# Kernel optimization log

Hardware: AMD Instinct MI355X
Metric: run time of the kernel (lower is better)

The kernel has to match this reference:

```python
import jax, jax.numpy as jnp
import numpy as np

N = 100000   # nodes
E = 3200000  # edges
G = 512      # graphs in batch
EPS = 1e-5   # batchnorm eps


def _lin(key, fan_in, fan_out):
    return jax.random.normal(key, (fan_in, fan_out), jnp.float32) / np.sqrt(fan_in)


def setup_inputs() -> dict:
    key = jax.random.key(0)
    ks = jax.random.split(key, 12)
    x = jax.random.normal(ks[0], (N, 2), jnp.float32)
    edge_index = jax.random.randint(ks[1], (2, E), 0, N, dtype=jnp.int64)
    batch_index = jnp.sort(jax.random.randint(ks[2], (N,), 0, G, dtype=jnp.int64))
    w = (8, 32, 128)
    return {
        "x": x, "edge_index": edge_index, "batch_index": batch_index,
        "W1": _lin(ks[3], 2, w[0]),   "b1": jnp.zeros((w[0],), jnp.float32),
        "g1": jnp.ones((w[0],), jnp.float32),  "be1": jnp.zeros((w[0],), jnp.float32),
        "W2": _lin(ks[4], w[0], w[1]), "b2": jnp.zeros((w[1],), jnp.float32),
        "g2": jnp.ones((w[1],), jnp.float32),  "be2": jnp.zeros((w[1],), jnp.float32),
        "W3": _lin(ks[5], w[1], w[2]), "b3": jnp.zeros((w[2],), jnp.float32),
        "g3": jnp.ones((w[2],), jnp.float32),  "be3": jnp.zeros((w[2],), jnp.float32),
        "Wl": _lin(ks[6], w[2], 3),    "bl": jnp.zeros((3,), jnp.float32),
    }


def _gcn_norm(edge_index):
    # add self loops, symmetric normalization (PyG GCNConv default)
    loops = jnp.arange(N, dtype=edge_index.dtype)
    src = jnp.concatenate([edge_index[0], loops])
    dst = jnp.concatenate([edge_index[1], loops])
    deg = jax.ops.segment_sum(jnp.ones_like(dst, jnp.float32), dst, num_segments=N)
    dis = jnp.where(deg > 0, jax.lax.rsqrt(jnp.maximum(deg, 1.0)), 0.0)
    norm = dis[src] * dis[dst]  # [E+N]
    return src, dst, norm


def _gcn_conv(h, W, b, src, dst, norm):
    h = h @ W                                   # [N, out]
    msg = h[src] * norm[:, None]                # gather + scale
    return jax.ops.segment_sum(msg, dst, num_segments=N) + b


def _bn(h, g, b):
    # training-mode batchnorm over node dim
    m = jnp.mean(h, axis=0)
    v = jnp.mean(jnp.square(h - m), axis=0)
    return (h - m) * jax.lax.rsqrt(v + EPS) * g + b


def reference(x, edge_index, batch_index, W1, b1, g1, be1, W2, b2, g2, be2,
              W3, b3, g3, be3, Wl, bl):
    src, dst, norm = _gcn_norm(edge_index)
    h = _bn(jax.nn.relu(_gcn_conv(x, W1, b1, src, dst, norm)), g1, be1)
    h = _bn(jax.nn.relu(_gcn_conv(h, W2, b2, src, dst, norm)), g2, be2)
    h = _bn(jax.nn.relu(_gcn_conv(h, W3, b3, src, dst, norm)), g3, be3)
    pooled = jax.ops.segment_max(h, batch_index, num_segments=G)  # [G, 128]
    logits = pooled @ Wl + bl                                     # [G, 3]
    return jax.nn.log_softmax(logits, axis=1)
```

## Files before the change

kernel.cpp:

```cpp
#include <hip/hip_runtime.h>
#include <hip/hip_bf16.h>
#include <hip/hip_fp16.h>
#include <math.h>

#define N_NODES 100000
#define N_EDGES 3200000
#define N_GRAPHS 512
#define BN_EPS 1e-5f
#define NBIN ((N_NODES + 511) / 512)
#define CHUNK 8192
#define NCHUNK ((N_EDGES + CHUNK - 1) / CHUNK)
#define STORE_CAP (N_EDGES + 16 * NBIN * NCHUNK)
#define LSEG 98
#define NSEGB ((N_NODES + LSEG - 1) / LSEG)
#define NMMB ((N_NODES + 63) / 64)
#define NB2 3125
#define NB2P 3136
#define PLANE2 ((size_t)(N_NODES + 1) * 16)
#define PLANEU ((size_t)N_NODES * 16)

typedef _Float16 half8_t __attribute__((ext_vector_type(8)));
typedef float float4_t __attribute__((ext_vector_type(4)));

struct alignas(8) h4 { __half2 a, b; };
struct alignas(16) h8s { __half2 h[4]; };


__global__ void k_hist2(const int* __restrict__ dst, int* __restrict__ hists) {
    __shared__ int h[NBIN];
    for (int i = threadIdx.x; i < NBIN; i += blockDim.x) h[i] = 0;
    __syncthreads();
    int e0 = blockIdx.x * CHUNK;
    int e1 = min(e0 + CHUNK, N_EDGES);
    for (int e = e0 + threadIdx.x; e < e1; e += blockDim.x)
        atomicAdd(&h[dst[e] >> 9], 1);
    __syncthreads();
    for (int i = threadIdx.x; i < NBIN; i += blockDim.x)
        hists[i * NCHUNK + blockIdx.x] = h[i];
}

__global__ void k_scan2(int* __restrict__ hists, int* __restrict__ ghist) {
    int b = blockIdx.x;
    int lane = threadIdx.x;
    int carry = 0;
    int base = b * NCHUNK;
    for (int c0 = 0; c0 < NCHUNK; c0 += 64) {
        int c = c0 + lane;
        int v = (c < NCHUNK) ? hists[base + c] : 0;
        int pv = (v + 15) & ~15;
        int inc = pv;
#pragma unroll
        for (int off = 1; off < 64; off <<= 1) {
            int u = __shfl_up(inc, off, 64);
            if (lane >= off) inc += u;
        }
        if (c < NCHUNK) hists[base + c] = inc - pv + carry;
        carry += __shfl(inc, 63, 64);
    }
    if (lane == 0) ghist[b] = carry;
}

__global__ void k_binscan(const int* __restrict__ ghist, int* __restrict__ bbase) {
    __shared__ int sd[512];
    int t = threadIdx.x;
    int v = (t < NBIN) ? ghist[t] : 0;
    sd[t] = v;
    __syncthreads();
    for (int off = 1; off < 512; off <<= 1) {
        int u = (t >= off) ? sd[t - off] : 0;
        __syncthreads();
        sd[t] += u;
        __syncthreads();
    }
    if (t < NBIN) bbase[t] = sd[t] - v;
    if (t == 511) bbase[NBIN] = sd[511];
}

__global__ void k_scatter(const int* __restrict__ src, const int* __restrict__ dst,
                          const int* __restrict__ bbase, const int* __restrict__ hists,
                          int* __restrict__ store) {
    __shared__ int cur[NBIN];
    for (int i = threadIdx.x; i < NBIN; i += blockDim.x)
        cur[i] = bbase[i] + hists[i * NCHUNK + blockIdx.x];
    __syncthreads();
    int e0 = blockIdx.x * CHUNK;
    int e1 = min(e0 + CHUNK, N_EDGES);
    for (int e = e0 + threadIdx.x; e < e1; e += blockDim.x) {
        int d = dst[e];
        int b = d >> 9;
        int pos = atomicAdd(&cur[b], 1);
        store[pos] = (src[e] << 9) | (d & 511);
    }
    __syncthreads();
    for (int i = threadIdx.x; i < NBIN; i += blockDim.x) {
        int p = cur[i];
        int end = (p + 15) & ~15;
        for (; p < end; ++p) store[p] = -1;
    }
}

__global__ void k_csr_build(const int* __restrict__ bbase, const int* __restrict__ store,
                            const float* __restrict__ x, int* __restrict__ offs,
                            int* __restrict__ ends, float* __restrict__ dis,
                            float* __restrict__ rdis, float4* __restrict__ xd,
                            int* __restrict__ csr) {
    __shared__ int cnt[512], cur[512], wsum[4];
    int b = blockIdx.x;
    int n0 = b << 9;
    int e0 = bbase[b], e1 = bbase[b + 1];
    int t = threadIdx.x;
    int lane = t & 63, wid = t >> 6;
    if (t < 512) cnt[t] = 0;
    __syncthreads();
    for (int e = e0 + t; e < e1; e += 1024) {
        int p = store[e];
        if (p >= 0) atomicAdd(&cnt[p & 511], 1);
    }
    __syncthreads();
    int c0 = 0, c1 = 0, pair = 0, inc = 0;
    if (t < 256) {
        c0 = cnt[2 * t];
        c1 = cnt[2 * t + 1];
        pair = c0 + c1;
        inc = pair;
#pragma unroll
        for (int off = 1; off < 64; off <<= 1) {
            int u = __shfl_up(inc, off, 64);
            if (lane >= off) inc += u;
        }
        if (lane == 63) wsum[wid] = inc;
    }
    __syncthreads();
    if (t < 256) {
        int wo = 0;
        for (int w = 0; w < wid; ++w) wo += wsum[w];
        int ex = inc - pair + wo;
        cur[2 * t] = ex;
        cur[2 * t + 1] = ex + c0;
#pragma unroll
        for (int j = 0; j < 2; ++j) {
            int n = n0 + 2 * t + j;
            int cc = j ? c1 : c0;
            int exx = j ? ex + c0 : ex;
            if (n < N_NODES) {
                offs[n] = e0 + exx;
                ends[n] = e0 + exx + cc;
                float dn = rsqrtf(1.0f + (float)cc);
                dis[n] = dn;
                rdis[n] = sqrtf(1.0f + (float)cc);
                float2 xv = *(const float2*)(x + 2 * (size_t)n);
                xd[n] = make_float4(dn * xv.x, dn * xv.y, dn, 0.f);
            } else if (n == N_NODES) {
                xd[N_NODES] = make_float4(0.f, 0.f, 0.f, 0.f);
            }
        }
    }
    __syncthreads();
    for (int e = e0 + t; e < e1; e += 1024) {
        int p = store[e];
        if (p >= 0) {
            int pos = e0 + atomicAdd(&cur[p & 511], 1);
            csr[pos] = p >> 9;
        }
    }
}


__global__ void k_agg1(const float4* __restrict__ xd, const int* __restrict__ offs,
                       const int* __restrict__ ends, const int* __restrict__ csr,
                       const float* __restrict__ W1, const float* __restrict__ b1,
                       float* __restrict__ svec, __half* __restrict__ ys1) {
    __shared__ float sW[16], sb[8];
    int t = threadIdx.x;
    if (t < 16) sW[t] = W1[t];
    if (t < 8) sb[t] = b1[t];
    __syncthreads();
    int wave = t >> 6, lane = t & 63;
    int nsub = lane >> 4, eg = lane & 15;
    int node = ((blockIdx.x * 4 + wave) << 2) + nsub;
    int e0 = offs[node], e1 = ends[node];
    float ax = 0.f, ay = 0.f, as = 0.f;
    for (int e = e0 + eg; e < e1; e += 64) {
        int s[4];
#pragma unroll
        for (int j = 0; j < 4; ++j)
            s[j] = (e + 16 * j < e1) ? csr[e + 16 * j] : N_NODES;
        float4 v[4];
#pragma unroll
        for (int j = 0; j < 4; ++j) v[j] = xd[s[j]];
#pragma unroll
        for (int j = 0; j < 4; ++j) {
            ax += v[j].x;
            ay += v[j].y;
            as += v[j].z;
        }
    }
#pragma unroll
    for (int off = 1; off < 16; off <<= 1) {
        ax += __shfl_xor(ax, off, 64);
        ay += __shfl_xor(ay, off, 64);
        as += __shfl_xor(as, off, 64);
    }
    if (eg == 0) {
        float4 xn = xd[node];
        float dn = xn.z;
        float u0x = dn * (ax + xn.x);
        float u0y = dn * (ay + xn.y);
        svec[node] = dn * (as + xn.z);
        float y[8];
#pragma unroll
        for (int f = 0; f < 8; ++f)
            y[f] = dn * fmaxf(u0x * sW[f] + u0y * sW[8 + f] + sb[f], 0.f);
        h8s o;
#pragma unroll
        for (int q = 0; q < 4; ++q) o.h[q] = __floats2half2_rn(y[2 * q], y[2 * q + 1]);
        *(h8s*)(ys1 + (size_t)node * 8) = o;
    }
}


__global__ void k_prep2(const float* __restrict__ stats, const float* __restrict__ gamma,
                        const float* __restrict__ beta, const float* __restrict__ W2,
                        float* __restrict__ W2p, float* __restrict__ cw2,
                        __half* __restrict__ ys1) {
    __shared__ float a1[8], c1[8];
    int t = threadIdx.x;
    if (t < 8) {
        float inv_n = 1.0f / (float)N_NODES;
        float m = stats[t] * inv_n;
        float v = stats[8 + t] * inv_n - m * m;
        float a = gamma[t] * rsqrtf(v + BN_EPS);
        a1[t] = a;
        c1[t] = beta[t] - m * a;
    }
    __syncthreads();
    W2p[t] = a1[t >> 5] * W2[t];
    if (t < 32) {
        float cb = 0.f;
#pragma unroll
        for (int i = 0; i < 8; ++i) cb += c1[i] * W2[i * 32 + t];
        cw2[t] = cb;
    }
    if (t == 128) *(int4*)(ys1 + (size_t)N_NODES * 8) = make_int4(0, 0, 0, 0);
}


__global__ void k_agg2(const __half* __restrict__ ys1, const int* __restrict__ offs,
                       const int* __restrict__ ends, const int* __restrict__ csr,
                       const float* __restrict__ dis, const float* __restrict__ svec,
                       const float* __restrict__ W2p, const float* __restrict__ cw2,
                       const float* __restrict__ b2, __half* __restrict__ ys2,
                       float* __restrict__ part2) {
    __shared__ float sW[256], sC[32], sB[32], sm2[64];
    int t = threadIdx.x;
    sW[t] = W2p[t];
    if (t < 32) { sC[t] = cw2[t]; sB[t] = b2[t]; }
    if (t < 64) sm2[t] = 0.f;
    __syncthreads();
    int wave = t >> 6, lane = t & 63;
    int nsub = lane >> 3, eg = (lane >> 1) & 3, chunk = lane & 1;
    int node = ((blockIdx.x * 4 + wave) << 3) + nsub;
    int e0 = offs[node], e1 = ends[node];
    float a0 = 0.f, a1 = 0.f, a2 = 0.f, a3 = 0.f;
    const __half* hp = ys1 + chunk * 4;
    for (int e = e0 + eg; e < e1; e += 16) {
        int s[4];
#pragma unroll
        for (int j = 0; j < 4; ++j)
            s[j] = (e + 4 * j < e1) ? csr[e + 4 * j] : N_NODES;
        h4 v[4];
#pragma unroll
        for (int j = 0; j < 4; ++j) v[j] = *(const h4*)(hp + (size_t)s[j] * 8);
#pragma unroll
        for (int j = 0; j < 4; ++j) {
            a0 += __low2float(v[j].a);
            a1 += __high2float(v[j].a);
            a2 += __low2float(v[j].b);
            a3 += __high2float(v[j].b);
        }
    }
    if (eg == 0) {
        h4 v = *(const h4*)(hp + (size_t)node * 8);
        a0 += __low2float(v.a);
        a1 += __high2float(v.a);
        a2 += __low2float(v.b);
        a3 += __high2float(v.b);
    }
#pragma unroll
    for (int off = 2; off < 8; off <<= 1) {
        a0 += __shfl_xor(a0, off, 64);
        a1 += __shfl_xor(a1, off, 64);
        a2 += __shfl_xor(a2, off, 64);
        a3 += __shfl_xor(a3, off, 64);
    }
    int lb = nsub << 3;
    float u[8];
    u[0] = __shfl(a0, lb, 64);     u[1] = __shfl(a1, lb, 64);
    u[2] = __shfl(a2, lb, 64);     u[3] = __shfl(a3, lb, 64);
    u[4] = __shfl(a0, lb + 1, 64); u[5] = __shfl(a1, lb + 1, 64);
    u[6] = __shfl(a2, lb + 1, 64); u[7] = __shfl(a3, lb + 1, 64);
    float dn = dis[node];
    float sv = svec[node];
#pragma unroll
    for (int i = 0; i < 8; ++i) u[i] *= dn;
    int c0 = (lane & 7) * 4;
    float hh[4], hs2[4];
#pragma unroll
    for (int k = 0; k < 4; ++k) {
        int col = c0 + k;
        float conv = sB[col] + sv * sC[col];
#pragma unroll
        for (int i = 0; i < 8; ++i) conv += u[i] * sW[i * 32 + col];
        hh[k] = fmaxf(conv, 0.f);
        hs2[k] = hh[k] * hh[k];
    }
    h4 o;
    o.a = __floats2half2_rn(dn * hh[0], dn * hh[1]);
    o.b = __floats2half2_rn(dn * hh[2], dn * hh[3]);
    *(h4*)(ys2 + (size_t)(c0 >> 4) * PLANE2 + (size_t)node * 16 + (c0 & 15)) = o;

    float hs[4];
#pragma unroll
    for (int k = 0; k < 4; ++k) hs[k] = hh[k];
#pragma unroll
    for (int off = 8; off < 64; off <<= 1)
#pragma unroll
        for (int k = 0; k < 4; ++k) {
            hs[k] += __shfl_xor(hs[k], off, 64);
            hs2[k] += __shfl_xor(hs2[k], off, 64);
        }
    if (nsub == 0) {
#pragma unroll
        for (int k = 0; k < 4; ++k) {
            atomicAdd(&sm2[c0 + k], hs[k]);
            atomicAdd(&sm2[32 + c0 + k], hs2[k]);
        }
    }
    __syncthreads();
    if (t < 64) part2[(size_t)t * NB2P + blockIdx.x] = sm2[t];
}

__global__ void k_red32(const float* __restrict__ part2, float* __restrict__ stats2) {
    int i = blockIdx.x;
    int t = threadIdx.x;
    float s = 0.f;
    for (int b = t; b < NB2; b += 256) s += part2[(size_t)i * NB2P + b];
    __shared__ float sm[256];
    sm[t] = s;
    __syncthreads();
    for (int st = 128; st > 0; st >>= 1) {
        if (t < st) sm[t] += sm[t + st];
        __syncthreads();
    }
    if (t == 0) stats2[i] = sm[0];
}


__global__ void k_prep3(const float* __restrict__ stats, const float* __restrict__ gamma,
                        const float* __restrict__ beta, const float* __restrict__ W3,
                        __half* __restrict__ wfrag, float* __restrict__ cw3,
                        __half* __restrict__ ys2) {
    __shared__ float a2[32], c2[32];
    int t = threadIdx.x;
    if (t < 32) {
        float inv_n = 1.0f / (float)N_NODES;
        float m = stats[t] * inv_n;
        float v = stats[32 + t] * inv_n - m * m;
        float a = gamma[t] * rsqrtf(v + BN_EPS);
        a2[t] = a;
        c2[t] = beta[t] - m * a;
    }
    __syncthreads();
    {
        int g = t >> 6, kq = (t >> 4) & 3, c = t & 15;
#pragma unroll
        for (int j = 0; j < 8; ++j) {
            int k = kq * 8 + j;
            wfrag[(size_t)t * 8 + j] = __float2half(a2[k] * W3[k * 128 + g * 16 + c]);
        }
    }
    if (t < 128) {
        float cb = 0.f;
#pragma unroll
        for (int k = 0; k < 32; ++k) cb += c2[k] * W3[k * 128 + t];
        cw3[t] = cb;
    }
    if (t >= 480 && t < 496) {
        int idx = t - 480;
        ((__half2*)(ys2 + (size_t)(idx >> 3) * PLANE2 + (size_t)N_NODES * 16))[idx & 7] =
            __half2{__float2half(0.f), __float2half(0.f)};
    }
}


__global__ void k_agg3(const __half* __restrict__ ys2, const int* __restrict__ offs,
                       const int* __restrict__ ends, const int* __restrict__ csr,
                       const float* __restrict__ dis, __half* __restrict__ u2, int plane) {
    int wave = threadIdx.x >> 6;
    int lane = threadIdx.x & 63;
    int nsub = lane >> 5;
    int eg = (lane >> 2) & 7;
    int chunk = lane & 3;
    int node = ((blockIdx.x * 4 + wave) << 1) + nsub;
    int e0 = offs[node], e1 = ends[node];
    float ax = 0.f, ay = 0.f, az = 0.f, aw = 0.f;
    const __half* hp = ys2 + (size_t)plane * PLANE2 + chunk * 4;
    for (int e = e0 + eg; e < e1; e += 64) {
        int s[8];
#pragma unroll
        for (int j = 0; j < 8; ++j)
            s[j] = (e + 8 * j < e1) ? csr[e + 8 * j] : N_NODES;
        h4 v[8];
#pragma unroll
        for (int j = 0; j < 8; ++j) v[j] = *(const h4*)(hp + (size_t)s[j] * 16);
#pragma unroll
        for (int j = 0; j < 8; ++j) {
            ax += __low2float(v[j].a);
            ay += __high2float(v[j].a);
            az += __low2float(v[j].b);
            aw += __high2float(v[j].b);
        }
    }
    if (eg == 0) {
        h4 v = *(const h4*)(hp + (size_t)node * 16);
        ax += __low2float(v.a);
        ay += __high2float(v.a);
        az += __low2float(v.b);
        aw += __high2float(v.b);
    }
#pragma unroll
    for (int off = 4; off < 32; off <<= 1) {
        ax += __shfl_xor(ax, off, 64);
        ay += __shfl_xor(ay, off, 64);
        az += __shfl_xor(az, off, 64);
        aw += __shfl_xor(aw, off, 64);
    }
    if (eg == 0) {
        float dn = dis[node];
        h4 o;
        o.a = __floats2half2_rn(dn * ax, dn * ay);
        o.b = __floats2half2_rn(dn * az, dn * aw);
        *(h4*)(u2 + (size_t)plane * PLANEU + (size_t)node * 16 + chunk * 4) = o;
    }
}


__global__ void k_mm_mfma(const __half* __restrict__ u2, const __half* __restrict__ wfrag,
                          const float* __restrict__ cw3, const float* __restrict__ b3,
                          const float* __restrict__ svec, const float* __restrict__ dis,
                          __half* __restrict__ ys3, float* __restrict__ spart) {
    __shared__ float sm[256];
    int t = threadIdx.x;
    int wave = t >> 6;
    int lane = t & 63;
    int n0 = (blockIdx.x * 4 + wave) * 16;
    bool active = n0 < N_NODES;
    int m = lane & 15;
    int kq = lane >> 4;
    float ss[8] = {0, 0, 0, 0, 0, 0, 0, 0};
    float ss2[8] = {0, 0, 0, 0, 0, 0, 0, 0};

    if (active) {
        half8_t af = *(const half8_t*)(u2 + (size_t)(kq >> 1) * PLANEU +
                                       (size_t)(n0 + m) * 16 + (kq & 1) * 8);
        float4_t accs[8];
#pragma unroll
        for (int g = 0; g < 8; ++g) {
            float4_t acc = {0.f, 0.f, 0.f, 0.f};
            half8_t bf = *(const half8_t*)(wfrag + (size_t)((g * 4 + kq) * 16 + m) * 8);
            accs[g] = __builtin_amdgcn_mfma_f32_16x16x32_f16(af, bf, acc, 0, 0, 0);
        }
        float sv[4], dn[4];
#pragma unroll
        for (int r = 0; r < 4; ++r) {
            sv[r] = svec[n0 + kq * 4 + r];
            dn[r] = dis[n0 + kq * 4 + r];
        }
#pragma unroll
        for (int g = 0; g < 8; ++g) {
            float cwf = cw3[g * 16 + m];
            float bf3 = b3[g * 16 + m];
#pragma unroll
            for (int r = 0; r < 4; ++r) {
                float y = fmaxf(accs[g][r] + sv[r] * cwf + bf3, 0.f);
                ss[g] += y;
                ss2[g] += y * y;
                ys3[(size_t)(n0 + kq * 4 + r) * 128 + g * 16 + m] = __float2half(dn[r] * y);
            }
        }
    }
#pragma unroll
    for (int off = 16; off < 64; off <<= 1)
#pragma unroll
        for (int g = 0; g < 8; ++g) {
            ss[g] += __shfl_xor(ss[g], off, 64);
            ss2[g] += __shfl_xor(ss2[g], off, 64);
        }
    sm[t] = 0.f;
    __syncthreads();
    if (active && kq == 0) {
#pragma unroll
        for (int g = 0; g < 8; ++g) {
            atomicAdd(&sm[g * 16 + m], ss[g]);
            atomicAdd(&sm[128 + g * 16 + m], ss2[g]);
        }
    }
    __syncthreads();
    spart[(size_t)blockIdx.x * 256 + t] = sm[t];
}


template <int FOUT>
__global__ void k_stats(const __half* __restrict__ ys, const float* __restrict__ rdis,
                        float* __restrict__ stats) {
    constexpr int GP = 256 / FOUT;
    int f = threadIdx.x % FOUT, g = threadIdx.x / FOUT;
    float s = 0.f, s2 = 0.f;
    for (int n = blockIdx.x * GP + g; n < N_NODES; n += gridDim.x * GP) {
        float v = __half2float(ys[(size_t)n * FOUT + f]) * rdis[n];
        s += v;
        s2 += v * v;
    }
    __shared__ float ls[256], ls2[256];
    ls[threadIdx.x] = s;
    ls2[threadIdx.x] = s2;
    __syncthreads();
    if (g == 0) {
        for (int gg = 1; gg < GP; ++gg) {
            s += ls[gg * FOUT + f];
            s2 += ls2[gg * FOUT + f];
        }
        atomicAdd(&stats[f], s);
        atomicAdd(&stats[FOUT + f], s2);
    }
}

__global__ void k_stats_red(const float* __restrict__ part, float* __restrict__ stats) {
    int i = blockIdx.x;
    int t = threadIdx.x;
    float s = 0.f;
    for (int b = t; b < NMMB; b += 256) s += part[(size_t)b * 256 + i];
    __shared__ float sm[256];
    sm[t] = s;
    __syncthreads();
    for (int st = 128; st > 0; st >>= 1) {
        if (t < st) sm[t] += sm[t + st];
        __syncthreads();
    }
    if (t == 0) stats[i] = sm[0];
}


__global__ void k_pool1(const __half* __restrict__ ys3, const float* __restrict__ rdis,
                        const int* __restrict__ batch, int* __restrict__ gmax,
                        int* __restrict__ gmin) {
    __shared__ int sb[LSEG];
    __shared__ float sr[LSEG];
    int n0 = blockIdx.x * LSEG;
    int n1 = min(n0 + LSEG, N_NODES);
    int L = n1 - n0;
    int f = threadIdx.x;
    for (int i = f; i < L; i += 128) { sb[i] = batch[n0 + i]; sr[i] = rdis[n0 + i]; }
    __syncthreads();
    if (L <= 0) return;
    int cg = sb[0];
    int mx = 0;
    int mn = 0x7F800000;
    for (int i = 0; i < L; ++i) {
        int g = sb[i];
        if (g != cg) {
            atomicMax(&gmax[cg * 128 + f], mx);
            atomicMin(&gmin[cg * 128 + f], mn);
            cg = g; mx = 0; mn = 0x7F800000;
        }
        float v = __half2float(ys3[(size_t)(n0 + i) * 128 + f]) * sr[i];
        int b = __float_as_int(v);
        mx = max(mx, b);
        mn = min(mn, b);
    }
    atomicMax(&gmax[cg * 128 + f], mx);
    atomicMin(&gmin[cg * 128 + f], mn);
}


__device__ __forceinline__ int lower_bound_dev(const int* __restrict__ a, int val) {
    int lo = 0, hi = N_NODES;
    while (lo < hi) {
        int mid = (lo + hi) >> 1;
        if (a[mid] < val) lo = mid + 1; else hi = mid;
    }
    return lo;
}

__global__ void k_poolhead(const int* __restrict__ gmax, const int* __restrict__ gmin,
                           const int* __restrict__ batch, const float* __restrict__ stats,
                           const float* __restrict__ gamma, const float* __restrict__ beta,
                           const float* __restrict__ Wl, const float* __restrict__ bl,
                           float* __restrict__ out) {
    int g = blockIdx.x;
    int f = threadIdx.x;
    float inv_n = 1.0f / (float)N_NODES;
    float m = stats[f] * inv_n;
    float var = stats[128 + f] * inv_n - m * m;
    float a = gamma[f] * rsqrtf(var + BN_EPS);
    float c = beta[f] - m * a;
    int s = lower_bound_dev(batch, g);
    int e = lower_bound_dev(batch, g + 1);
    float mx = __int_as_float(gmax[g * 128 + f]);
    float mn = __int_as_float(gmin[g * 128 + f]);
    float r;
    if (e > s) r = (a >= 0.f) ? (a * mx + c) : (a * mn + c);
    else r = -INFINITY;
    __shared__ float l[3][128];
    l[0][f] = r * Wl[f * 3 + 0];
    l[1][f] = r * Wl[f * 3 + 1];
    l[2][f] = r * Wl[f * 3 + 2];
    __syncthreads();
    for (int st = 64; st > 0; st >>= 1) {
        if (f < st) {
            l[0][f] += l[0][f + st];
            l[1][f] += l[1][f + st];
            l[2][f] += l[2][f + st];
        }
        __syncthreads();
    }
    if (f == 0) {
        float l0 = l[0][0] + bl[0], l1 = l[1][0] + bl[1], l2 = l[2][0] + bl[2];
        float mxl = fmaxf(l0, fmaxf(l1, l2));
        float lse = mxl + logf(expf(l0 - mxl) + expf(l1 - mxl) + expf(l2 - mxl));
        out[g * 3 + 0] = l0 - lse;
        out[g * 3 + 1] = l1 - lse;
        out[g * 3 + 2] = l2 - lse;
    }
}


extern "C" void kernel_launch(void* const* d_in, const int* in_sizes, int n_in,
                              void* d_out, int out_size, void* d_ws, size_t ws_size,
                              hipStream_t stream) {
    const float* x   = (const float*)d_in[0];
    const int* ei    = (const int*)d_in[1];
    const int* src   = ei;
    const int* dst   = ei + N_EDGES;
    const int* batch = (const int*)d_in[2];
    const float *W1 = (const float*)d_in[3],  *b1 = (const float*)d_in[4];
    const float *g1 = (const float*)d_in[5],  *be1 = (const float*)d_in[6];
    const float *W2 = (const float*)d_in[7],  *b2 = (const float*)d_in[8];
    const float *g2 = (const float*)d_in[9],  *be2 = (const float*)d_in[10];
    const float *W3 = (const float*)d_in[11], *b3 = (const float*)d_in[12];
    const float *g3 = (const float*)d_in[13], *be3 = (const float*)d_in[14];
    const float *Wl = (const float*)d_in[15], *bl = (const float*)d_in[16];
    float* out = (float*)d_out;

    int* base = (int*)d_ws;
    size_t o = 0;
    float* stats1 = (float*)(base + o); o += 256;
    float* stats2 = (float*)(base + o); o += 256;
    float* stats3 = (float*)(base + o); o += 256;
    int* gmax     = base + o; o += (size_t)N_GRAPHS * 128;
    size_t zero_words = o;
    int* gmin     = base + o; o += (size_t)N_GRAPHS * 128;
    int* bbase    = base + o; o += NBIN + 4;
    int* ghist    = base + o; o += NBIN + 4;
    int* hists    = base + o; o += ((size_t)NBIN * NCHUNK + 3) & ~3ULL;
    float* W2p    = (float*)(base + o); o += 256;
    float* cw2    = (float*)(base + o); o += 32;
    __half* wfrag = (__half*)(base + o); o += 2048;
    float* cw3    = (float*)(base + o); o += 128;
    int* offs     = base + o; o += 100000;
    int* ends     = base + o; o += 100000;
    int* store    = base + o; o += STORE_CAP;
    int* csr      = base + o; o += STORE_CAP;
    float* dis    = (float*)(base + o); o += N_NODES;
    float* rdis   = (float*)(base + o); o += N_NODES;
    float* svec   = (float*)(base + o); o += N_NODES;
    float* spart  = (float*)(base + o); o += (size_t)NMMB * 256;
    float* part2  = (float*)(base + o); o += (size_t)64 * NB2P;
    float4* xd    = (float4*)(base + o); o += (size_t)(N_NODES + 1) * 4;
    __half* ys1   = (__half*)(base + o); o += (size_t)(N_NODES + 1) * 4;
    __half* ys2   = (__half*)(base + o); o += (size_t)(N_NODES + 1) * 16;
    __half* u2    = (__half*)(base + o); o += (size_t)N_NODES * 16;
    __half* ys3   = (__half*)(base + o); o += (size_t)N_NODES * 64;
    if (ws_size < o * 4) return;

    const int TB = 256;

    hipMemsetAsync(base, 0, zero_words * 4, stream);
    hipMemsetAsync(gmin, 0x7F, (size_t)N_GRAPHS * 128 * 4, stream);

    k_hist2<<<NCHUNK, 1024, 0, stream>>>(dst, hists);
    k_scan2<<<NBIN, 64, 0, stream>>>(hists, ghist);
    k_binscan<<<1, 512, 0, stream>>>(ghist, bbase);
    k_scatter<<<NCHUNK, 1024, 0, stream>>>(src, dst, bbase, hists, store);
    k_csr_build<<<NBIN, 1024, 0, stream>>>(bbase, store, x, offs, ends, dis, rdis, xd, csr);

    k_agg1<<<N_NODES / 16, TB, 0, stream>>>(xd, offs, ends, csr, W1, b1, svec, ys1);
    k_stats<8><<<256, 256, 0, stream>>>(ys1, rdis, stats1);
    k_prep2<<<1, 256, 0, stream>>>(stats1, g1, be1, W2, W2p, cw2, ys1);

    k_agg2<<<NB2, TB, 0, stream>>>(ys1, offs, ends, csr, dis, svec, W2p, cw2, b2, ys2, part2);
    k_red32<<<64, 256, 0, stream>>>(part2, stats2);
    k_prep3<<<1, 512, 0, stream>>>(stats2, g2, be2, W3, wfrag, cw3, ys2);

    k_agg3<<<N_NODES / 8, TB, 0, stream>>>(ys2, offs, ends, csr, dis, u2, 0);
    k_agg3<<<N_NODES / 8, TB, 0, stream>>>(ys2, offs, ends, csr, dis, u2, 1);
    k_mm_mfma<<<NMMB, 256, 0, stream>>>(u2, wfrag, cw3, b3, svec, dis, ys3, spart);
    k_stats_red<<<256, 256, 0, stream>>>(spart, stats3);

    k_pool1<<<NSEGB, 128, 0, stream>>>(ys3, rdis, batch, gmax, gmin);
    k_poolhead<<<N_GRAPHS, 128, 0, stream>>>(gmax, gmin, batch, stats3, g3, be3, Wl, bl, out);
}
```

Measured before the change: 359.2 us.

## Vectorize edge loads, batch store reads, merge agg3 launches, vectorize stats

Loads dst/src as int4 pairs in the histogram and scatter kernels, and batches four store reads per thread in csr_build before issuing the shared atomics. Replaces the generic stats kernel for layer 1 with one that reads eight halves per node and reduces them with wave shuffles. Merges the two per-plane agg3 launches into one grid that picks the plane from blockIdx, and prefetches eight ys3 values ahead in pool1. The goal is fewer memory transactions, more loads in flight and less launch overhead. The scatter changes the order edges land in each bin, so the CSR neighbour order and the floating-point summation order change.

Measured after the change: 323.7 us. -9.9%, faster.

```diff
diff --git a/kernel.cpp b/kernel.cpp
--- a/kernel.cpp
+++ b/kernel.cpp
@@ -32,8 +32,17 @@
     __syncthreads();
     int e0 = blockIdx.x * CHUNK;
     int e1 = min(e0 + CHUNK, N_EDGES);
-    for (int e = e0 + threadIdx.x; e < e1; e += blockDim.x)
-        atomicAdd(&h[dst[e] >> 9], 1);
+    int e = e0 + threadIdx.x * 8;
+    if (e + 8 <= e1) {
+        int4 d0 = *(const int4*)(dst + e);
+        int4 d1 = *(const int4*)(dst + e + 4);
+        atomicAdd(&h[d0.x >> 9], 1); atomicAdd(&h[d0.y >> 9], 1);
+        atomicAdd(&h[d0.z >> 9], 1); atomicAdd(&h[d0.w >> 9], 1);
+        atomicAdd(&h[d1.x >> 9], 1); atomicAdd(&h[d1.y >> 9], 1);
+        atomicAdd(&h[d1.z >> 9], 1); atomicAdd(&h[d1.w >> 9], 1);
+    } else {
+        for (; e < e1; ++e) atomicAdd(&h[dst[e] >> 9], 1);
+    }
     __syncthreads();
     for (int i = threadIdx.x; i < NBIN; i += blockDim.x)
         hists[i * NCHUNK + blockIdx.x] = h[i];
@@ -85,11 +94,26 @@
     __syncthreads();
     int e0 = blockIdx.x * CHUNK;
     int e1 = min(e0 + CHUNK, N_EDGES);
-    for (int e = e0 + threadIdx.x; e < e1; e += blockDim.x) {
-        int d = dst[e];
-        int b = d >> 9;
-        int pos = atomicAdd(&cur[b], 1);
-        store[pos] = (src[e] << 9) | (d & 511);
+    int e = e0 + threadIdx.x * 8;
+    if (e + 8 <= e1) {
+        int4 d0 = *(const int4*)(dst + e), d1 = *(const int4*)(dst + e + 4);
+        int4 s0 = *(const int4*)(src + e), s1 = *(const int4*)(src + e + 4);
+        int dd[8] = {d0.x, d0.y, d0.z, d0.w, d1.x, d1.y, d1.z, d1.w};
+        int sv[8] = {s0.x, s0.y, s0.z, s0.w, s1.x, s1.y, s1.z, s1.w};
+#pragma unroll
+        for (int j = 0; j < 8; ++j) {
+            int d = dd[j];
+            int b = d >> 9;
+            int pos = atomicAdd(&cur[b], 1);
+            store[pos] = (sv[j] << 9) | (d & 511);
+        }
+    } else {
+        for (; e < e1; ++e) {
+            int d = dst[e];
+            int b = d >> 9;
+            int pos = atomicAdd(&cur[b], 1);
+            store[pos] = (src[e] << 9) | (d & 511);
+        }
     }
     __syncthreads();
     for (int i = threadIdx.x; i < NBIN; i += blockDim.x) {
@@ -112,9 +136,14 @@
     int lane = t & 63, wid = t >> 6;
     if (t < 512) cnt[t] = 0;
     __syncthreads();
-    for (int e = e0 + t; e < e1; e += 1024) {
-        int p = store[e];
-        if (p >= 0) atomicAdd(&cnt[p & 511], 1);
+    for (int e = e0 + t; e < e1; e += 4096) {
+        int p[4];
+#pragma unroll
+        for (int j = 0; j < 4; ++j)
+            p[j] = (e + 1024 * j < e1) ? store[e + 1024 * j] : -1;
+#pragma unroll
+        for (int j = 0; j < 4; ++j)
+            if (p[j] >= 0) atomicAdd(&cnt[p[j] & 511], 1);
     }
     __syncthreads();
     int c0 = 0, c1 = 0, pair = 0, inc = 0;
@@ -156,12 +185,17 @@
         }
     }
     __syncthreads();
-    for (int e = e0 + t; e < e1; e += 1024) {
-        int p = store[e];
-        if (p >= 0) {
-            int pos = e0 + atomicAdd(&cur[p & 511], 1);
-            csr[pos] = p >> 9;
-        }
+    for (int e = e0 + t; e < e1; e += 4096) {
+        int p[4];
+#pragma unroll
+        for (int j = 0; j < 4; ++j)
+            p[j] = (e + 1024 * j < e1) ? store[e + 1024 * j] : -1;
+#pragma unroll
+        for (int j = 0; j < 4; ++j)
+            if (p[j] >= 0) {
+                int pos = e0 + atomicAdd(&cur[p[j] & 511], 1);
+                csr[pos] = p[j] >> 9;
+            }
     }
 }
 
@@ -216,6 +250,44 @@
         for (int q = 0; q < 4; ++q) o.h[q] = __floats2half2_rn(y[2 * q], y[2 * q + 1]);
         *(h8s*)(ys1 + (size_t)node * 8) = o;
     }
+}
+
+
+__global__ void k_stats8v(const __half* __restrict__ ys1, const float* __restrict__ rdis,
+                          float* __restrict__ stats) {
+    int t = threadIdx.x;
+    float s[8] = {0, 0, 0, 0, 0, 0, 0, 0};
+    float s2[8] = {0, 0, 0, 0, 0, 0, 0, 0};
+    for (int n = blockIdx.x * 256 + t; n < N_NODES; n += gridDim.x * 256) {
+        float r = rdis[n];
+        h8s v = *(const h8s*)(ys1 + (size_t)n * 8);
+#pragma unroll
+        for (int q = 0; q < 4; ++q) {
+            float v0 = __low2float(v.h[q]) * r;
+            float v1 = __high2float(v.h[q]) * r;
+            s[2 * q] += v0;      s2[2 * q] += v0 * v0;
+            s[2 * q + 1] += v1;  s2[2 * q + 1] += v1 * v1;
+        }
+    }
+#pragma unroll
+    for (int off = 1; off < 64; off <<= 1)
+#pragma unroll
+        for (int k = 0; k < 8; ++k) {
+            s[k] += __shfl_xor(s[k], off, 64);
+            s2[k] += __shfl_xor(s2[k], off, 64);
+        }
+    __shared__ float sm[16];
+    if (t < 16) sm[t] = 0.f;
+    __syncthreads();
+    if ((t & 63) == 0) {
+#pragma unroll
+        for (int k = 0; k < 8; ++k) {
+            atomicAdd(&sm[k], s[k]);
+            atomicAdd(&sm[8 + k], s2[k]);
+        }
+    }
+    __syncthreads();
+    if (t < 16) atomicAdd(&stats[t], sm[t]);
 }
 
 
@@ -395,13 +467,15 @@
 
 __global__ void k_agg3(const __half* __restrict__ ys2, const int* __restrict__ offs,
                        const int* __restrict__ ends, const int* __restrict__ csr,
-                       const float* __restrict__ dis, __half* __restrict__ u2, int plane) {
+                       const float* __restrict__ dis, __half* __restrict__ u2) {
+    int plane = blockIdx.x & 1;
+    int nb = blockIdx.x >> 1;
     int wave = threadIdx.x >> 6;
     int lane = threadIdx.x & 63;
     int nsub = lane >> 5;
     int eg = (lane >> 2) & 7;
     int chunk = lane & 3;
-    int node = ((blockIdx.x * 4 + wave) << 1) + nsub;
+    int node = ((nb * 4 + wave) << 1) + nsub;
     int e0 = offs[node], e1 = ends[node];
     float ax = 0.f, ay = 0.f, az = 0.f, aw = 0.f;
     const __half* hp = ys2 + (size_t)plane * PLANE2 + chunk * 4;
@@ -507,32 +581,6 @@
     }
     __syncthreads();
     spart[(size_t)blockIdx.x * 256 + t] = sm[t];
-}
-
-
-template <int FOUT>
-__global__ void k_stats(const __half* __restrict__ ys, const float* __restrict__ rdis,
-                        float* __restrict__ stats) {
-    constexpr int GP = 256 / FOUT;
-    int f = threadIdx.x % FOUT, g = threadIdx.x / FOUT;
-    float s = 0.f, s2 = 0.f;
-    for (int n = blockIdx.x * GP + g; n < N_NODES; n += gridDim.x * GP) {
-        float v = __half2float(ys[(size_t)n * FOUT + f]) * rdis[n];
-        s += v;
-        s2 += v * v;
-    }
-    __shared__ float ls[256], ls2[256];
-    ls[threadIdx.x] = s;
-    ls2[threadIdx.x] = s2;
-    __syncthreads();
-    if (g == 0) {
-        for (int gg = 1; gg < GP; ++gg) {
-            s += ls[gg * FOUT + f];
-            s2 += ls2[gg * FOUT + f];
-        }
-        atomicAdd(&stats[f], s);
-        atomicAdd(&stats[FOUT + f], s2);
-    }
 }
 
 __global__ void k_stats_red(const float* __restrict__ part, float* __restrict__ stats) {
@@ -566,17 +614,27 @@
     int cg = sb[0];
     int mx = 0;
     int mn = 0x7F800000;
-    for (int i = 0; i < L; ++i) {
-        int g = sb[i];
-        if (g != cg) {
-            atomicMax(&gmax[cg * 128 + f], mx);
-            atomicMin(&gmin[cg * 128 + f], mn);
-            cg = g; mx = 0; mn = 0x7F800000;
-        }
-        float v = __half2float(ys3[(size_t)(n0 + i) * 128 + f]) * sr[i];
-        int b = __float_as_int(v);
-        mx = max(mx, b);
-        mn = min(mn, b);
+    for (int i0 = 0; i0 < L; i0 += 8) {
+        int lim = min(8, L - i0);
+        __half v[8];
+#pragma unroll
+        for (int j = 0; j < 8; ++j)
+            if (j < lim) v[j] = ys3[(size_t)(n0 + i0 + j) * 128 + f];
+#pragma unroll
+        for (int j = 0; j < 8; ++j) {
+            if (j >= lim) break;
+            int i = i0 + j;
+            int g = sb[i];
+            if (g != cg) {
+                atomicMax(&gmax[cg * 128 + f], mx);
+                atomicMin(&gmin[cg * 128 + f], mn);
+                cg = g; mx = 0; mn = 0x7F800000;
+            }
+            float val = __half2float(v[j]) * sr[i];
+            int b = __float_as_int(val);
+            mx = max(mx, b);
+            mn = min(mn, b);
+        }
     }
     atomicMax(&gmax[cg * 128 + f], mx);
     atomicMin(&gmin[cg * 128 + f], mn);
@@ -695,15 +753,14 @@
     k_csr_build<<<NBIN, 1024, 0, stream>>>(bbase, store, x, offs, ends, dis, rdis, xd, csr);
 
     k_agg1<<<N_NODES / 16, TB, 0, stream>>>(xd, offs, ends, csr, W1, b1, svec, ys1);
-    k_stats<8><<<256, 256, 0, stream>>>(ys1, rdis, stats1);
+    k_stats8v<<<64, 256, 0, stream>>>(ys1, rdis, stats1);
     k_prep2<<<1, 256, 0, stream>>>(stats1, g1, be1, W2, W2p, cw2, ys1);
 
     k_agg2<<<NB2, TB, 0, stream>>>(ys1, offs, ends, csr, dis, svec, W2p, cw2, b2, ys2, part2);
     k_red32<<<64, 256, 0, stream>>>(part2, stats2);
     k_prep3<<<1, 512, 0, stream>>>(stats2, g2, be2, W3, wfrag, cw3, ys2);
 
-    k_agg3<<<N_NODES / 8, TB, 0, stream>>>(ys2, offs, ends, csr, dis, u2, 0);
-    k_agg3<<<N_NODES / 8, TB, 0, stream>>>(ys2, offs, ends, csr, dis, u2, 1);
+    k_agg3<<<2 * (N_NODES / 8), TB, 0, stream>>>(ys2, offs, ends, csr, dis, u2);
     k_mm_mfma<<<NMMB, 256, 0, stream>>>(u2, wfrag, cw3, b3, svec, dis, ys3, spart);
     k_stats_red<<<256, 256, 0, stream>>>(spart, stats3);
 
```
